# Kernel optimization log

Measured on AMD Instinct MI355X. Metric: run time of the kernel, lower is better.

The kernel has to match this reference:

```python
import jax, jax.numpy as jnp
import numpy as np

HID = 24

def setup_inputs() -> dict:
    key = jax.random.key(0)
    ks = jax.random.split(key, 20)
    B, T = 1024, 4096
    s = 0.1
    inp = {
        "x": jax.random.normal(ks[0], (B, T, 1), jnp.float32),
        "h": jnp.zeros((3, B, HID), jnp.float32),
        # RNN layer 0 (input size 1)
        "W_ih0": jax.random.normal(ks[1], (HID, 1), jnp.float32) * s,
        "b_ih0": jax.random.normal(ks[2], (HID,), jnp.float32) * s,
        "W_hh0": jax.random.normal(ks[3], (HID, HID), jnp.float32) * s,
        "b_hh0": jax.random.normal(ks[4], (HID,), jnp.float32) * s,
        # RNN layer 1
        "W_ih1": jax.random.normal(ks[5], (HID, HID), jnp.float32) * s,
        "b_ih1": jax.random.normal(ks[6], (HID,), jnp.float32) * s,
        "W_hh1": jax.random.normal(ks[7], (HID, HID), jnp.float32) * s,
        "b_hh1": jax.random.normal(ks[8], (HID,), jnp.float32) * s,
        # RNN layer 2
        "W_ih2": jax.random.normal(ks[9], (HID, HID), jnp.float32) * s,
        "b_ih2": jax.random.normal(ks[10], (HID,), jnp.float32) * s,
        "W_hh2": jax.random.normal(ks[11], (HID, HID), jnp.float32) * s,
        "b_hh2": jax.random.normal(ks[12], (HID,), jnp.float32) * s,
        # MLP head 24 -> 24 -> 1
        "W1": jax.random.normal(ks[13], (HID, HID), jnp.float32) * s,
        "b1": jax.random.normal(ks[14], (HID,), jnp.float32) * s,
        "W2": jax.random.normal(ks[15], (1, HID), jnp.float32) * s,
        "b2": jax.random.normal(ks[16], (1,), jnp.float32) * s,
    }
    return inp


def reference(x, h,
              W_ih0, b_ih0, W_hh0, b_hh0,
              W_ih1, b_ih1, W_hh1, b_hh1,
              W_ih2, b_ih2, W_hh2, b_hh2,
              W1, b1, W2, b2):
    # x: [B, T, 1]; h: [3, B, 24]. force=True -> every step uses x[:, i, :];
    # returned y is the MLP output of the LAST timestep only.
    relu = jax.nn.relu

    def cell(carry, x_t):  # x_t: [B, 1]
        h0, h1, h2 = carry
        h0n = relu(x_t @ W_ih0.T + b_ih0 + h0 @ W_hh0.T + b_hh0)
        h1n = relu(h0n @ W_ih1.T + b_ih1 + h1 @ W_hh1.T + b_hh1)
        h2n = relu(h1n @ W_ih2.T + b_ih2 + h2 @ W_hh2.T + b_hh2)
        y = relu(relu(h2n @ W1.T + b1) @ W2.T + b2)  # [B, 1]
        return (h0n, h1n, h2n), y

    xs = jnp.swapaxes(x, 0, 1)  # [T, B, 1]
    (h0f, h1f, h2f), ys = jax.lax.scan(cell, (h[0], h[1], h[2]), xs)
    y = ys[-1]                       # [B, 1]
    h_final = jnp.stack([h0f, h1f, h2f])  # [3, B, 24]
    return y, h_final
```

## Files before the change

### kernel.cpp

```cpp
#include <hip/hip_runtime.h>

#define HID   24
#define T_LEN 4096
#define BATCH 1024
#define NB    2
#define K     32
#define NC    (T_LEN / K)
#define CTOT  (NC + 2)
#define TPB   192
#define PS    32

typedef __attribute__((ext_vector_type(2))) _Float16 h2v;
typedef __attribute__((ext_vector_type(4))) int      int4v;

#if __has_builtin(__builtin_amdgcn_fdot2)
__device__ __forceinline__ float dot2f(int p, int w, float acc) {
    return __builtin_amdgcn_fdot2(__builtin_bit_cast(h2v, p),
                                  __builtin_bit_cast(h2v, w), acc, false);
}
#else
__device__ __forceinline__ float dot2f(int p, int w, float acc) {
    h2v a = __builtin_bit_cast(h2v, p), b = __builtin_bit_cast(h2v, w);
    acc = fmaf((float)a.x, (float)b.x, acc);
    return fmaf((float)a.y, (float)b.y, acc);
}
#endif

__device__ __forceinline__ float dot4(const float4 a, const float4 b, float acc) {
    acc = fmaf(a.x, b.x, acc);
    acc = fmaf(a.y, b.y, acc);
    acc = fmaf(a.z, b.z, acc);
    return fmaf(a.w, b.w, acc);
}

#define PKF(A_, B_)                                                                 \
    (((int)__builtin_bit_cast(unsigned short, (_Float16)(B_)) << 16) |              \
     (int)__builtin_bit_cast(unsigned short, (_Float16)(A_)))

__global__ __launch_bounds__(TPB, 1) void rnn_bal_kernel(
    const float* __restrict__ x,
    const float* __restrict__ h_in,
    const float* __restrict__ Wih0, const float* __restrict__ bih0,
    const float* __restrict__ Whh0, const float* __restrict__ bhh0,
    const float* __restrict__ Wih1, const float* __restrict__ bih1,
    const float* __restrict__ Whh1, const float* __restrict__ bhh1,
    const float* __restrict__ Wih2, const float* __restrict__ bih2,
    const float* __restrict__ Whh2, const float* __restrict__ bhh2,
    const float* __restrict__ W1,   const float* __restrict__ b1,
    const float* __restrict__ W2,   const float* __restrict__ b2,
    float* __restrict__ out)
{
    __shared__ __align__(16) _Float16 row0[2][NB][PS];
    __shared__ __align__(16) _Float16 row2[2][NB][PS];
    __shared__ __align__(16) _Float16 pub1[2][NB][K][PS];
    __shared__ __align__(16) float part1[2][NB][K][PS];
    __shared__ float h2f[NB][HID];
    __shared__ float mbuf[NB][HID];

    const int tid  = threadIdx.x;
    const int l    = tid >> 6;
    const int lane = tid & 63;
    const int bl   = lane >> 5;
    const int jj   = lane & 31;
    const bool act = (jj < HID);
    const int uL   = act ? jj : (jj - 8);
    const int bg   = blockIdx.x * NB + bl;

    int4v whA, whB, whC;
    int4v wiA = {0,0,0,0}, wiB = {0,0,0,0}, wiC = {0,0,0,0};
    float wx0 = 0.f, bias;

#define MK3(ROW, DA, DB, DC) do {                                                   \
        DA = (int4v){PKF((ROW)[0], (ROW)[1]),   PKF((ROW)[2], (ROW)[3]),            \
                     PKF((ROW)[4], (ROW)[5]),   PKF((ROW)[6], (ROW)[7])};           \
        DB = (int4v){PKF((ROW)[8], (ROW)[9]),   PKF((ROW)[10], (ROW)[11]),          \
                     PKF((ROW)[12], (ROW)[13]), PKF((ROW)[14], (ROW)[15])};         \
        DC = (int4v){PKF((ROW)[16], (ROW)[17]), PKF((ROW)[18], (ROW)[19]),          \
                     PKF((ROW)[20], (ROW)[21]), PKF((ROW)[22], (ROW)[23])};         \
    } while (0)

    if (l == 0) {
        MK3(Whh0 + uL * HID, whA, whB, whC);
        MK3(Wih1 + uL * HID, wiA, wiB, wiC);
        wx0  = Wih0[uL];
        bias = bih0[uL] + bhh0[uL];
    } else if (l == 1) {
        MK3(Whh1 + uL * HID, whA, whB, whC);
        bias = bih1[uL] + bhh1[uL];
    } else {
        MK3(Whh2 + uL * HID, whA, whB, whC);
        MK3(Wih2 + uL * HID, wiA, wiB, wiC);
        bias = bih2[uL] + bhh2[uL];
    }
#undef MK3

    float cur = h_in[(l * BATCH + bg) * HID + uL];

    if (l == 0) row0[1][bl][jj] = (_Float16)cur;
    if (l == 1) pub1[0][bl][K - 1][jj] = (_Float16)cur;
    if (l == 2) row2[1][bl][jj] = (_Float16)cur;

    const float* xrow = x + (size_t)bg * T_LEN;
    float4 xq[8], xn[8];
    if (l == 0) {
        const float4* xr = (const float4*)xrow;
        #pragma unroll
        for (int q = 0; q < 8; ++q) xq[q] = xr[q];
    }
#define XV(S)                                                                       \
    (((S) & 3) == 0 ? xq[(S) >> 2].x : ((S) & 3) == 1 ? xq[(S) >> 2].y              \
   : ((S) & 3) == 2 ? xq[(S) >> 2].z : xq[(S) >> 2].w)

#define DOT12(V0_, V1_, V2_, W0_, W1_, W2_, A0_, A1_)                               \
    A0_ = dot2f(V0_.x, W0_.x, A0_); A1_ = dot2f(V0_.y, W0_.y, A1_);                 \
    A0_ = dot2f(V0_.z, W0_.z, A0_); A1_ = dot2f(V0_.w, W0_.w, A1_);                 \
    A0_ = dot2f(V1_.x, W1_.x, A0_); A1_ = dot2f(V1_.y, W1_.y, A1_);                 \
    A0_ = dot2f(V1_.z, W1_.z, A0_); A1_ = dot2f(V1_.w, W1_.w, A1_);                 \
    A0_ = dot2f(V2_.x, W2_.x, A0_); A1_ = dot2f(V2_.y, W2_.y, A1_);                 \
    A0_ = dot2f(V2_.z, W2_.z, A0_); A1_ = dot2f(V2_.w, W2_.w, A1_);

    __syncthreads();

    for (int c = 0; c < CTOT; ++c) {
        const int wp = c & 1, rp = wp ^ 1;
        if (l == 0) {
            if (c < NC) {
                const bool pf = (c + 1 < NC);
                if (pf) {
                    const float4* xr = (const float4*)(xrow + (size_t)(c + 1) * K);
                    #pragma unroll
                    for (int q = 0; q < 8; ++q) xn[q] = xr[q];
                }
                #pragma unroll
                for (int s = 0; s < K; ++s) {
                    const int4v* own = (const int4v*)&row0[(s + 1) & 1][bl][0];
                    const int4v o0 = own[0], o1 = own[1], o2 = own[2];
                    float a0 = fmaf(wx0, XV(s), bias), a1 = 0.f;
                    DOT12(o0, o1, o2, whA, whB, whC, a0, a1);
                    cur = fmaxf(a0 + a1, 0.f);
                    row0[s & 1][bl][jj] = (_Float16)cur;
                    if (s > 0) {
                        float p0 = 0.f, p1 = 0.f;
                        DOT12(o0, o1, o2, wiA, wiB, wiC, p0, p1);
                        part1[wp][bl][s - 1][jj] = p0 + p1;
                    }
                }
                {
                    const int4v* own = (const int4v*)&row0[1][bl][0];
                    const int4v o0 = own[0], o1 = own[1], o2 = own[2];
                    float p0 = 0.f, p1 = 0.f;
                    DOT12(o0, o1, o2, wiA, wiB, wiC, p0, p1);
                    part1[wp][bl][K - 1][jj] = p0 + p1;
                }
                if (pf) {
                    #pragma unroll
                    for (int q = 0; q < 8; ++q) xq[q] = xn[q];
                }
            }
        } else if (l == 1) {
            if (c >= 1 && c < 1 + NC) {
                #pragma unroll
                for (int s = 0; s < K; ++s) {
                    const int4v* own = (s == 0)
                        ? (const int4v*)&pub1[rp][bl][K - 1][0]
                        : (const int4v*)&pub1[wp][bl][s - 1][0];
                    const int4v o0 = own[0], o1 = own[1], o2 = own[2];
                    const float pin = part1[rp][bl][s][jj];
                    float a0 = pin + bias, a1 = 0.f;
                    DOT12(o0, o1, o2, whA, whB, whC, a0, a1);
                    cur = fmaxf(a0 + a1, 0.f);
                    pub1[wp][bl][s][jj] = (_Float16)cur;
                }
            }
        } else {
            if (c >= 2 && c < 2 + NC) {
                const int4v* src = (const int4v*)&pub1[rp][bl][0][0];
                int4v iA0 = src[0], iA1 = src[1], iA2 = src[2];
                #pragma unroll
                for (int s = 0; s < K; ++s) {
                    int4v iB0, iB1, iB2;
                    if (s + 1 < K) {
                        const int4v* nr = (const int4v*)&pub1[rp][bl][s + 1][0];
                        iB0 = nr[0]; iB1 = nr[1]; iB2 = nr[2];
                    }
                    const int4v* own = (const int4v*)&row2[(s + 1) & 1][bl][0];
                    const int4v o0 = own[0], o1 = own[1], o2 = own[2];
                    float a0 = bias, a1 = 0.f, a2 = 0.f, a3 = 0.f;
                    DOT12(iA0, iA1, iA2, wiA, wiB, wiC, a0, a1);
                    DOT12(o0, o1, o2, whA, whB, whC, a2, a3);
                    cur = fmaxf((a0 + a1) + (a2 + a3), 0.f);
                    row2[s & 1][bl][jj] = (_Float16)cur;
                    if (s + 1 < K) { iA0 = iB0; iA1 = iB1; iA2 = iB2; }
                }
            }
        }
        __syncthreads();
    }
#undef XV
#undef DOT12

    if (act) out[BATCH + (size_t)(l * BATCH + bg) * HID + uL] = cur;

    if (l == 2 && act) h2f[bl][uL] = cur;
    __syncthreads();
    if (l == 2 && act) {
        const float4* w1r = (const float4*)(W1 + uL * HID);
        const float4* hv  = (const float4*)&h2f[bl][0];
        float a = b1[uL];
        a = dot4(w1r[0], hv[0], a); a = dot4(w1r[1], hv[1], a);
        a = dot4(w1r[2], hv[2], a); a = dot4(w1r[3], hv[3], a);
        a = dot4(w1r[4], hv[4], a); a = dot4(w1r[5], hv[5], a);
        mbuf[bl][uL] = fmaxf(a, 0.f);
    }
    __syncthreads();
    if (l == 2 && jj == 0) {
        float a = b2[0];
        #pragma unroll
        for (int k = 0; k < HID; ++k) a = fmaf(W2[k], mbuf[bl][k], a);
        out[bg] = fmaxf(a, 0.f);
    }
}

extern "C" void kernel_launch(void* const* d_in, const int* in_sizes, int n_in,
                              void* d_out, int out_size, void* d_ws, size_t ws_size,
                              hipStream_t stream) {
    const float* x    = (const float*)d_in[0];
    const float* h_in = (const float*)d_in[1];
    const float* Wih0 = (const float*)d_in[2];
    const float* bih0 = (const float*)d_in[3];
    const float* Whh0 = (const float*)d_in[4];
    const float* bhh0 = (const float*)d_in[5];
    const float* Wih1 = (const float*)d_in[6];
    const float* bih1 = (const float*)d_in[7];
    const float* Whh1 = (const float*)d_in[8];
    const float* bhh1 = (const float*)d_in[9];
    const float* Wih2 = (const float*)d_in[10];
    const float* bih2 = (const float*)d_in[11];
    const float* Whh2 = (const float*)d_in[12];
    const float* bhh2 = (const float*)d_in[13];
    const float* W1   = (const float*)d_in[14];
    const float* b1   = (const float*)d_in[15];
    const float* W2   = (const float*)d_in[16];
    const float* b2   = (const float*)d_in[17];
    float* out = (float*)d_out;

    dim3 grid(BATCH / NB);
    dim3 block(TPB);
    hipLaunchKernelGGL(rnn_bal_kernel, grid, block, 0, stream,
                       x, h_in, Wih0, bih0, Whh0, bhh0,
                       Wih1, bih1, Whh1, bhh1, Wih2, bih2, Whh2, bhh2,
                       W1, b1, W2, b2, out);
}
```

Before: 510.4 us.

## Move layer-2 input projection into layer-1 wave to rebalance pipeline stages

Layer 1 now computes the Wih2 projection of its own fresh hidden state off the critical path, one step lagged in the same style as layer 0 does for Wih1. It writes those partial sums to a new float buffer part2 that layer 2 reads. Layer 2 therefore runs only the recurrent Whh2 dot per step instead of two 24-wide dots. The three waves get more even per-step work, which shortens the slowest stage in the wavefront pipeline. The cost is more shared memory for part2 and more work in layer 1.

```diff
diff --git a/kernel.cpp b/kernel.cpp
--- a/kernel.cpp
+++ b/kernel.cpp
@@ -37,7 +37,7 @@
     (((int)__builtin_bit_cast(unsigned short, (_Float16)(B_)) << 16) |              \
      (int)__builtin_bit_cast(unsigned short, (_Float16)(A_)))
 
-__global__ __launch_bounds__(TPB, 1) void rnn_bal_kernel(
+__global__ __launch_bounds__(TPB, 1) void rnn_bal2_kernel(
     const float* __restrict__ x,
     const float* __restrict__ h_in,
     const float* __restrict__ Wih0, const float* __restrict__ bih0,
@@ -51,9 +51,10 @@
     float* __restrict__ out)
 {
     __shared__ __align__(16) _Float16 row0[2][NB][PS];
+    __shared__ __align__(16) _Float16 row1[2][NB][PS];
     __shared__ __align__(16) _Float16 row2[2][NB][PS];
-    __shared__ __align__(16) _Float16 pub1[2][NB][K][PS];
     __shared__ __align__(16) float part1[2][NB][K][PS];
+    __shared__ __align__(16) float part2[2][NB][K][PS];
     __shared__ float h2f[NB][HID];
     __shared__ float mbuf[NB][HID];
 
@@ -86,10 +87,10 @@
         bias = bih0[uL] + bhh0[uL];
     } else if (l == 1) {
         MK3(Whh1 + uL * HID, whA, whB, whC);
+        MK3(Wih2 + uL * HID, wiA, wiB, wiC);
         bias = bih1[uL] + bhh1[uL];
     } else {
         MK3(Whh2 + uL * HID, whA, whB, whC);
-        MK3(Wih2 + uL * HID, wiA, wiB, wiC);
         bias = bih2[uL] + bhh2[uL];
     }
 #undef MK3
@@ -97,7 +98,7 @@
     float cur = h_in[(l * BATCH + bg) * HID + uL];
 
     if (l == 0) row0[1][bl][jj] = (_Float16)cur;
-    if (l == 1) pub1[0][bl][K - 1][jj] = (_Float16)cur;
+    if (l == 1) row1[1][bl][jj] = (_Float16)cur;
     if (l == 2) row2[1][bl][jj] = (_Float16)cur;
 
     const float* xrow = x + (size_t)bg * T_LEN;
@@ -131,6 +132,7 @@
                     #pragma unroll
                     for (int q = 0; q < 8; ++q) xn[q] = xr[q];
                 }
+                float* dst = &part1[wp][bl][0][0];
                 #pragma unroll
                 for (int s = 0; s < K; ++s) {
                     const int4v* own = (const int4v*)&row0[(s + 1) & 1][bl][0];
@@ -142,7 +144,7 @@
                     if (s > 0) {
                         float p0 = 0.f, p1 = 0.f;
                         DOT12(o0, o1, o2, wiA, wiB, wiC, p0, p1);
-                        part1[wp][bl][s - 1][jj] = p0 + p1;
+                        dst[(s - 1) * PS + jj] = p0 + p1;
                     }
                 }
                 {
@@ -150,7 +152,7 @@
                     const int4v o0 = own[0], o1 = own[1], o2 = own[2];
                     float p0 = 0.f, p1 = 0.f;
                     DOT12(o0, o1, o2, wiA, wiB, wiC, p0, p1);
-                    part1[wp][bl][K - 1][jj] = p0 + p1;
+                    dst[(K - 1) * PS + jj] = p0 + p1;
                 }
                 if (pf) {
                     #pragma unroll
@@ -159,38 +161,43 @@
             }
         } else if (l == 1) {
             if (c >= 1 && c < 1 + NC) {
+                const float* srcp = &part1[rp][bl][0][0];
+                float* dstp = &part2[wp][bl][0][0];
                 #pragma unroll
                 for (int s = 0; s < K; ++s) {
-                    const int4v* own = (s == 0)
-                        ? (const int4v*)&pub1[rp][bl][K - 1][0]
-                        : (const int4v*)&pub1[wp][bl][s - 1][0];
-                    const int4v o0 = own[0], o1 = own[1], o2 = own[2];
-                    const float pin = part1[rp][bl][s][jj];
+                    const int4v* own = (const int4v*)&row1[(s + 1) & 1][bl][0];
+                    const int4v o0 = own[0], o1 = own[1], o2 = own[2];
+                    const float pin = srcp[s * PS + jj];
                     float a0 = pin + bias, a1 = 0.f;
                     DOT12(o0, o1, o2, whA, whB, whC, a0, a1);
                     cur = fmaxf(a0 + a1, 0.f);
-                    pub1[wp][bl][s][jj] = (_Float16)cur;
+                    row1[s & 1][bl][jj] = (_Float16)cur;
+                    if (s > 0) {
+                        float p0 = 0.f, p1 = 0.f;
+                        DOT12(o0, o1, o2, wiA, wiB, wiC, p0, p1);
+                        dstp[(s - 1) * PS + jj] = p0 + p1;
+                    }
+                }
+                {
+                    const int4v* own = (const int4v*)&row1[1][bl][0];
+                    const int4v o0 = own[0], o1 = own[1], o2 = own[2];
+                    float p0 = 0.f, p1 = 0.f;
+                    DOT12(o0, o1, o2, wiA, wiB, wiC, p0, p1);
+                    dstp[(K - 1) * PS + jj] = p0 + p1;
                 }
             }
         } else {
             if (c >= 2 && c < 2 + NC) {
-                const int4v* src = (const int4v*)&pub1[rp][bl][0][0];
-                int4v iA0 = src[0], iA1 = src[1], iA2 = src[2];
+                const float* srcp = &part2[rp][bl][0][0];
                 #pragma unroll
                 for (int s = 0; s < K; ++s) {
-                    int4v iB0, iB1, iB2;
-                    if (s + 1 < K) {
-                        const int4v* nr = (const int4v*)&pub1[rp][bl][s + 1][0];
-                        iB0 = nr[0]; iB1 = nr[1]; iB2 = nr[2];
-                    }
                     const int4v* own = (const int4v*)&row2[(s + 1) & 1][bl][0];
                     const int4v o0 = own[0], o1 = own[1], o2 = own[2];
-                    float a0 = bias, a1 = 0.f, a2 = 0.f, a3 = 0.f;
-                    DOT12(iA0, iA1, iA2, wiA, wiB, wiC, a0, a1);
-                    DOT12(o0, o1, o2, whA, whB, whC, a2, a3);
-                    cur = fmaxf((a0 + a1) + (a2 + a3), 0.f);
+                    const float pin = srcp[s * PS + jj];
+                    float a0 = pin + bias, a1 = 0.f;
+                    DOT12(o0, o1, o2, whA, whB, whC, a0, a1);
+                    cur = fmaxf(a0 + a1, 0.f);
                     row2[s & 1][bl][jj] = (_Float16)cur;
-                    if (s + 1 < K) { iA0 = iB0; iA1 = iB1; iA2 = iB2; }
                 }
             }
         }
@@ -246,7 +253,7 @@
 
     dim3 grid(BATCH / NB);
     dim3 block(TPB);
-    hipLaunchKernelGGL(rnn_bal_kernel, grid, block, 0, stream,
+    hipLaunchKernelGGL(rnn_bal2_kernel, grid, block, 0, stream,
                        x, h_in, Wih0, bih0, Whh0, bhh0,
                        Wih1, bih1, Whh1, bhh1, Wih2, bih2, Whh2, bhh2,
                        W1, b1, W2, b2, out);
```

Result: slower. 576.4 us (+12.9%).
